# Optimization experiments

Measured on AMD Instinct MI355X. Metric: run time of the kernel, lower is better.

## Reference

```python
import jax, jax.numpy as jnp
import numpy as np

B, N, K, D, H = 4, 256, 32, 32, 8
NUM_SPATIAL, NUM_EDGES = 512, 1024


def setup_inputs() -> dict:
    key = jax.random.key(0)
    k1, k2, k3, k4, k5 = jax.random.split(key, 5)
    spatial_pos = jax.random.randint(k1, (B, N, N), 0, NUM_SPATIAL, dtype=jnp.int64)
    edge_input = jax.random.randint(k2, (B, N, N, K), 0, NUM_EDGES + 1, dtype=jnp.int64)
    spatial_emb = jax.random.normal(k3, (NUM_SPATIAL, H), dtype=jnp.float32)
    spatial_emb = spatial_emb.at[0].set(0.0)  # padding_idx=0
    edge_feat_emb = jax.random.normal(k4, (NUM_EDGES + 1, D), dtype=jnp.float32)
    edge_feat_emb = edge_feat_emb.at[0].set(0.0)  # padding_idx=0
    edge_pos_emb = jax.random.normal(k5, (K, D * H), dtype=jnp.float32)
    return {"spatial_pos": spatial_pos, "edge_input": edge_input,
            "spatial_emb": spatial_emb, "edge_feat_emb": edge_feat_emb,
            "edge_pos_emb": edge_pos_emb}


def reference(spatial_pos, edge_input, spatial_emb, edge_feat_emb, edge_pos_emb):
    # spatial bias: gather [B,N,N,H] -> [B,H,N,N]
    spatial_bias = jnp.transpose(spatial_emb[spatial_pos], (0, 3, 1, 2))
    # edge feature gather: [B,N,N,K,D]
    edge_feat = edge_feat_emb[edge_input]
    pos_weight = edge_pos_emb.reshape(K, D, H)  # [K,D,H]
    # per-hop projection then mean over valid hops
    terms = jnp.einsum('bnmkd,kdh->bnmkh', edge_feat, pos_weight)  # [B,N,N,K,H]
    mask = (edge_input != 0)
    path_len = jnp.maximum(mask.sum(axis=-1, keepdims=True).astype(terms.dtype), 1.0)  # [B,N,N,1]
    edge_bias = terms.sum(axis=-2) / path_len  # [B,N,N,H]
    edge_bias = jnp.transpose(edge_bias, (0, 3, 1, 2))  # [B,H,N,N]
    return spatial_bias + edge_bias
```

## Files before the change

### kernel.cpp

```cpp
#include <hip/hip_runtime.h>
#include <hip/hip_bf16.h>

#define BB 4
#define NN 256
#define KK 32
#define DD 32
#define HH 8
#define NROWS 1024
#define NPTS (BB * NN * NN)
#define NNSQ (NN * NN)
#define TPB 1024
#define NBLK (NPTS / TPB)
#define NPH 16
#define SLICE_US (NROWS * HH)
#define IPAD 4

typedef __attribute__((ext_vector_type(8))) unsigned short ushort8;
typedef __attribute__((ext_vector_type(4))) int iv4;
typedef __attribute__((ext_vector_type(4))) float fv4;

#define LGKM0 asm volatile("s_waitcnt lgkmcnt(0)" ::: "memory")
#define BAR   __builtin_amdgcn_s_barrier()

__device__ __forceinline__ unsigned short f2bf(float f) {
    unsigned u = __float_as_uint(f);
    unsigned r = (u + 0x7FFFu + ((u >> 16) & 1u)) >> 16;
    return (unsigned short)r;
}

__global__ __launch_bounds__(256) void build_proj_bf16(
    const float* __restrict__ feat,
    const float* __restrict__ w,
    unsigned short* __restrict__ proj)
{
    int t  = blockIdx.x * 256 + threadIdx.x;
    int k  = t >> 10;
    int e  = (t & 1023) + 1;

    const float* frow = feat + (size_t)e * DD;
    const float* wrow = w + (size_t)k * DD * HH;

    float acc[HH];
#pragma unroll
    for (int h = 0; h < HH; ++h) acc[h] = 0.0f;

#pragma unroll
    for (int d = 0; d < DD; ++d) {
        float f = frow[d];
#pragma unroll
        for (int h = 0; h < HH; ++h) acc[h] = fmaf(f, wrow[d * HH + h], acc[h]);
    }

    ushort8 o;
#pragma unroll
    for (int h = 0; h < HH; ++h) o[h] = f2bf(acc[h]);
    *(ushort8*)(proj + (size_t)t * HH) = o;
}

template <int E>
__global__ __launch_bounds__(TPB) void attn_bias_v6(
    const int* __restrict__ sp,
    const int* __restrict__ ei,
    const float* __restrict__ semb,
    const unsigned short* __restrict__ proj,
    float* __restrict__ out)
{
    __shared__ __align__(16) unsigned short tbuf[2][2 * SLICE_US];
    __shared__ unsigned int ibuf[2][4][NROWS + IPAD];

    const int tid = threadIdx.x;
    const int p0  = blockIdx.x * TPB;

    const fv4* P4  = (const fv4*)proj;
    const iv4* EI4 = (const iv4*)ei;
    const size_t bi4 = (size_t)p0 * (8 * E);

    fv4 S0, S1;
    iv4 cv[4];

    auto issueS = [&](int ph) {
        S0 = P4[(size_t)(2 * ph)     * 1024 + tid];
        S1 = P4[(size_t)(2 * ph + 1) * 1024 + tid];
    };
    auto writeS = [&](int nb) {
        *(fv4*)&tbuf[nb][tid * 8]            = S0;
        *(fv4*)&tbuf[nb][SLICE_US + tid * 8] = S1;
    };
    auto issueC = [&](int g) {
        if (E == 2) {
#pragma unroll
            for (int c = 0; c < 4; ++c) {
                int j = c * TPB + tid, pt = j >> 2, q = j & 3;
                cv[c] = EI4[bi4 + (size_t)pt * 16 + 4 * g + q];
            }
        } else {
#pragma unroll
            for (int c = 0; c < 2; ++c) {
                int j = c * TPB + tid, pt = j >> 1, q = j & 1;
                cv[c] = EI4[bi4 + (size_t)pt * 8 + 2 * g + q];
            }
        }
    };
    auto writeC = [&](int nb) {
        if (E == 2) {
#pragma unroll
            for (int c = 0; c < 4; ++c) {
                int j = c * TPB + tid, pt = j >> 2, q = j & 3;
                unsigned pk = ((unsigned)cv[c].x & 0xffffu) |
                              (((unsigned)cv[c].z & 0xffffu) << 16);
                ibuf[nb][q][pt] = pk;
            }
        } else {
#pragma unroll
            for (int c = 0; c < 2; ++c) {
                int j = c * TPB + tid, pt = j >> 1, q = j & 1;
                ibuf[nb][q * 2][pt] = ((unsigned)cv[c].x & 0xffffu) |
                                      (((unsigned)cv[c].y & 0xffffu) << 16);
                ibuf[nb][q * 2 + 1][pt] = ((unsigned)cv[c].z & 0xffffu) |
                                          (((unsigned)cv[c].w & 0xffffu) << 16);
            }
        }
    };

    issueS(0);
    issueC(0);
    const int pg = p0 + tid;
    int s = (E == 2) ? (int)((const long long*)sp)[pg] : sp[pg];

    writeS(0);
    issueS(1);
    writeC(0);
    issueC(1);
    LGKM0;
    BAR;

    float acc[HH];
#pragma unroll
    for (int h = 0; h < HH; ++h) acc[h] = 0.0f;
    int cnt = 0;

#pragma unroll 1
    for (int ph = 0; ph < NPH; ++ph) {
        const int g = ph >> 2;

        unsigned pr = ibuf[g & 1][ph & 3][tid];
        int e0 = pr & 0xffffu;
        int e1 = pr >> 16;
        int r0 = e0 ? (e0 - 1) : 0;
        int r1 = e1 ? (e1 - 1) : 0;
        float m0 = e0 ? 1.0f : 0.0f;
        float m1 = e1 ? 1.0f : 0.0f;
        cnt += (e0 != 0) + (e1 != 0);

        const unsigned short* tb = tbuf[ph & 1];
        ushort8 w0 = *(const ushort8*)&tb[r0 * 8];
        ushort8 w1 = *(const ushort8*)&tb[SLICE_US + r1 * 8];
#pragma unroll
        for (int h = 0; h < HH; ++h) {
            acc[h] = fmaf(m0, __uint_as_float(((unsigned)w0[h]) << 16), acc[h]);
            acc[h] = fmaf(m1, __uint_as_float(((unsigned)w1[h]) << 16), acc[h]);
        }

        if (ph < NPH - 1) {
            writeS((ph + 1) & 1);
            if (ph < NPH - 2) issueS(ph + 2);
            if ((ph & 3) == 3 && ph < 12) {
                writeC((g + 1) & 1);
                if (ph < 8) issueC(g + 2);
            }
            LGKM0;
            BAR;
        }
    }

    const float4* srow = (const float4*)(semb + (size_t)s * HH);
    float4 s0v = srow[0], s1v = srow[1];
    float sb[HH] = {s0v.x, s0v.y, s0v.z, s0v.w, s1v.x, s1v.y, s1v.z, s1v.w};

    float inv = 1.0f / (float)(cnt ? cnt : 1);
    float* o = out + (size_t)(pg >> 16) * (HH * NNSQ) + (pg & (NNSQ - 1));
#pragma unroll
    for (int h = 0; h < HH; ++h)
        o[(size_t)h * NNSQ] = sb[h] + acc[h] * inv;
}

extern "C" void kernel_launch(void* const* d_in, const int* in_sizes, int n_in,
                              void* d_out, int out_size, void* d_ws, size_t ws_size,
                              hipStream_t stream) {
    const int*   sp = (const int*)d_in[0];
    const int*   ei = (const int*)d_in[1];
    const float* se = (const float*)d_in[2];
    const float* fe = (const float*)d_in[3];
    const float* pw = (const float*)d_in[4];
    float* out = (float*)d_out;

    const bool i64 = (in_sizes[0] == 2 * NPTS);
    unsigned short* proj = (unsigned short*)d_ws;

    build_proj_bf16<<<128, 256, 0, stream>>>(fe, pw, proj);

    if (i64) attn_bias_v6<2><<<NBLK, TPB, 0, stream>>>(sp, ei, se, proj, out);
    else     attn_bias_v6<1><<<NBLK, TPB, 0, stream>>>(sp, ei, se, proj, out);
}
```

Measured before the change: 27.50 us.

## Stage projection slices via direct global-to-LDS loads with triple-buffered pipeline

Replaces the register-staged double-buffered projection table copy with global_load_lds direct-to-LDS loads into a three-slot ring, fully unrolling the 16 phases with explicit vmcnt waits. Padding hops now read from a shared zero row instead of a mask multiply, so the FMAs become plain adds. The aim is to cut register round-trips and LDS write instructions and to keep more loads in flight per barrier. In exchange it depends on hand-counted vmcnt values, which are fragile if the compiler reorders or adds memory operations.

```diff
diff --git a/kernel.cpp b/kernel.cpp
--- a/kernel.cpp
+++ b/kernel.cpp
@@ -11,21 +11,28 @@
 #define NNSQ (NN * NN)
 #define TPB 1024
 #define NBLK (NPTS / TPB)
-#define NPH 16
 #define SLICE_US (NROWS * HH)
-#define IPAD 4
+#define SLOT_US  (2 * SLICE_US)
 
 typedef __attribute__((ext_vector_type(8))) unsigned short ushort8;
 typedef __attribute__((ext_vector_type(4))) int iv4;
-typedef __attribute__((ext_vector_type(4))) float fv4;
-
-#define LGKM0 asm volatile("s_waitcnt lgkmcnt(0)" ::: "memory")
-#define BAR   __builtin_amdgcn_s_barrier()
+
+#define FENCE  asm volatile("" ::: "memory")
+#define LGKM0  asm volatile("s_waitcnt lgkmcnt(0)" ::: "memory")
+#define BAR    __builtin_amdgcn_s_barrier()
+#define VMW(n) asm volatile("s_waitcnt vmcnt(" #n ")" ::: "memory")
 
 __device__ __forceinline__ unsigned short f2bf(float f) {
     unsigned u = __float_as_uint(f);
     unsigned r = (u + 0x7FFFu + ((u >> 16) & 1u)) >> 16;
     return (unsigned short)r;
+}
+
+__device__ __forceinline__ void gload16(const void* g, void* l) {
+    __builtin_amdgcn_global_load_lds(
+        (const __attribute__((address_space(1))) void*)g,
+        (__attribute__((address_space(3))) void*)l,
+        16, 0, 0);
 }
 
 __global__ __launch_bounds__(256) void build_proj_bf16(
@@ -58,122 +65,120 @@
 }
 
 template <int E>
-__global__ __launch_bounds__(TPB) void attn_bias_v6(
+__global__ __launch_bounds__(TPB) void attn_bias_v8(
     const int* __restrict__ sp,
     const int* __restrict__ ei,
     const float* __restrict__ semb,
     const unsigned short* __restrict__ proj,
     float* __restrict__ out)
 {
-    __shared__ __align__(16) unsigned short tbuf[2][2 * SLICE_US];
-    __shared__ unsigned int ibuf[2][4][NROWS + IPAD];
+    __shared__ __align__(16) unsigned short tbuf[3 * SLOT_US];
+    __shared__ __align__(16) unsigned short zrow[8];
+    __shared__ unsigned int ibuf[2][4][NROWS + 4];
 
     const int tid = threadIdx.x;
     const int p0  = blockIdx.x * TPB;
-
-    const fv4* P4  = (const fv4*)proj;
+    const int pg  = p0 + tid;
+
+    constexpr int NC = (E == 2) ? 4 : 2;
     const iv4* EI4 = (const iv4*)ei;
     const size_t bi4 = (size_t)p0 * (8 * E);
 
-    fv4 S0, S1;
-    iv4 cv[4];
-
-    auto issueS = [&](int ph) {
-        S0 = P4[(size_t)(2 * ph)     * 1024 + tid];
-        S1 = P4[(size_t)(2 * ph + 1) * 1024 + tid];
-    };
-    auto writeS = [&](int nb) {
-        *(fv4*)&tbuf[nb][tid * 8]            = S0;
-        *(fv4*)&tbuf[nb][SLICE_US + tid * 8] = S1;
-    };
+    iv4 cv[NC];
+
     auto issueC = [&](int g) {
-        if (E == 2) {
-#pragma unroll
-            for (int c = 0; c < 4; ++c) {
+#pragma unroll
+        for (int c = 0; c < NC; ++c) {
+            if (E == 2) {
                 int j = c * TPB + tid, pt = j >> 2, q = j & 3;
                 cv[c] = EI4[bi4 + (size_t)pt * 16 + 4 * g + q];
-            }
-        } else {
-#pragma unroll
-            for (int c = 0; c < 2; ++c) {
+            } else {
                 int j = c * TPB + tid, pt = j >> 1, q = j & 1;
                 cv[c] = EI4[bi4 + (size_t)pt * 8 + 2 * g + q];
             }
         }
     };
     auto writeC = [&](int nb) {
-        if (E == 2) {
-#pragma unroll
-            for (int c = 0; c < 4; ++c) {
+#pragma unroll
+        for (int c = 0; c < NC; ++c) {
+            if (E == 2) {
                 int j = c * TPB + tid, pt = j >> 2, q = j & 3;
-                unsigned pk = ((unsigned)cv[c].x & 0xffffu) |
-                              (((unsigned)cv[c].z & 0xffffu) << 16);
-                ibuf[nb][q][pt] = pk;
-            }
-        } else {
-#pragma unroll
-            for (int c = 0; c < 2; ++c) {
+                ibuf[nb][q][pt] = ((unsigned)cv[c].x & 0xffffu) |
+                                  ((unsigned)cv[c].z << 16);
+            } else {
                 int j = c * TPB + tid, pt = j >> 1, q = j & 1;
-                ibuf[nb][q * 2][pt] = ((unsigned)cv[c].x & 0xffffu) |
-                                      (((unsigned)cv[c].y & 0xffffu) << 16);
-                ibuf[nb][q * 2 + 1][pt] = ((unsigned)cv[c].z & 0xffffu) |
-                                          (((unsigned)cv[c].w & 0xffffu) << 16);
+                ibuf[nb][2 * q][pt] = ((unsigned)cv[c].x & 0xffffu) |
+                                      ((unsigned)cv[c].y << 16);
+                ibuf[nb][2 * q + 1][pt] = ((unsigned)cv[c].z & 0xffffu) |
+                                          ((unsigned)cv[c].w << 16);
             }
         }
     };
-
-    issueS(0);
+    auto stage2 = [&](int phn, int slot) {
+        gload16(proj + (size_t)(2 * phn) * SLICE_US + tid * HH,
+                &tbuf[slot * SLOT_US + tid * HH]);
+        gload16(proj + (size_t)(2 * phn + 1) * SLICE_US + tid * HH,
+                &tbuf[slot * SLOT_US + SLICE_US + tid * HH]);
+    };
+
+    float acc[HH];
+#pragma unroll
+    for (int h = 0; h < HH; ++h) acc[h] = 0.0f;
+    int cnt = 0;
+
+    auto dohops = [&](int slot, int gsel, int q) {
+        unsigned pr = ibuf[gsel][q][tid];
+        int e0 = pr & 0xffffu;
+        int e1 = pr >> 16;
+        cnt += (e0 != 0) + (e1 != 0);
+        const unsigned short* tb = &tbuf[slot * SLOT_US];
+        const unsigned short* a0 = e0 ? tb + (e0 - 1) * HH : zrow;
+        const unsigned short* a1 = e1 ? tb + SLICE_US + (e1 - 1) * HH : zrow;
+        ushort8 w0 = *(const ushort8*)a0;
+        ushort8 w1 = *(const ushort8*)a1;
+#pragma unroll
+        for (int h = 0; h < HH; ++h) {
+            acc[h] += __uint_as_float(((unsigned)w0[h]) << 16);
+            acc[h] += __uint_as_float(((unsigned)w1[h]) << 16);
+        }
+    };
+
+#define VMWA do { if constexpr (E == 2) VMW(6); else VMW(4); } while (0)
+#define ENDPH do { FENCE; VMW(2); LGKM0; BAR; } while (0)
+
+    int sv = (E == 2) ? (int)((const long long*)sp)[pg] : sp[pg];
+    FENCE;
     issueC(0);
-    const int pg = p0 + tid;
-    int s = (E == 2) ? (int)((const long long*)sp)[pg] : sp[pg];
-
-    writeS(0);
-    issueS(1);
+    FENCE;
+    stage2(0, 0);
+    stage2(1, 1);
+    if (tid == 0) *(float4*)zrow = make_float4(0.f, 0.f, 0.f, 0.f);
+    FENCE;
     writeC(0);
     issueC(1);
-    LGKM0;
-    BAR;
-
-    float acc[HH];
-#pragma unroll
-    for (int h = 0; h < HH; ++h) acc[h] = 0.0f;
-    int cnt = 0;
-
-#pragma unroll 1
-    for (int ph = 0; ph < NPH; ++ph) {
-        const int g = ph >> 2;
-
-        unsigned pr = ibuf[g & 1][ph & 3][tid];
-        int e0 = pr & 0xffffu;
-        int e1 = pr >> 16;
-        int r0 = e0 ? (e0 - 1) : 0;
-        int r1 = e1 ? (e1 - 1) : 0;
-        float m0 = e0 ? 1.0f : 0.0f;
-        float m1 = e1 ? 1.0f : 0.0f;
-        cnt += (e0 != 0) + (e1 != 0);
-
-        const unsigned short* tb = tbuf[ph & 1];
-        ushort8 w0 = *(const ushort8*)&tb[r0 * 8];
-        ushort8 w1 = *(const ushort8*)&tb[SLICE_US + r1 * 8];
-#pragma unroll
-        for (int h = 0; h < HH; ++h) {
-            acc[h] = fmaf(m0, __uint_as_float(((unsigned)w0[h]) << 16), acc[h]);
-            acc[h] = fmaf(m1, __uint_as_float(((unsigned)w1[h]) << 16), acc[h]);
-        }
-
-        if (ph < NPH - 1) {
-            writeS((ph + 1) & 1);
-            if (ph < NPH - 2) issueS(ph + 2);
-            if ((ph & 3) == 3 && ph < 12) {
-                writeC((g + 1) & 1);
-                if (ph < 8) issueC(g + 2);
-            }
-            LGKM0;
-            BAR;
-        }
-    }
-
-    const float4* srow = (const float4*)(semb + (size_t)s * HH);
+    FENCE;
+    VMWA; LGKM0; BAR;
+
+    stage2(2, 2);  FENCE; dohops(0, 0, 0); FENCE; VMWA; LGKM0; BAR;
+    stage2(3, 0);  FENCE; dohops(1, 0, 1); ENDPH;
+    stage2(4, 1);  FENCE; dohops(2, 0, 2); ENDPH;
+    stage2(5, 2);  FENCE; dohops(0, 0, 3); writeC(1); issueC(2);
+                   FENCE; VMWA; LGKM0; BAR;
+    stage2(6, 0);  FENCE; dohops(1, 1, 0); FENCE; VMWA; LGKM0; BAR;
+    stage2(7, 1);  FENCE; dohops(2, 1, 1); ENDPH;
+    stage2(8, 2);  FENCE; dohops(0, 1, 2); ENDPH;
+    stage2(9, 0);  FENCE; dohops(1, 1, 3); writeC(0); issueC(3);
+                   FENCE; VMWA; LGKM0; BAR;
+    stage2(10, 1); FENCE; dohops(2, 0, 0); FENCE; VMWA; LGKM0; BAR;
+    stage2(11, 2); FENCE; dohops(0, 0, 1); ENDPH;
+    stage2(12, 0); FENCE; dohops(1, 0, 2); ENDPH;
+    stage2(13, 1); FENCE; dohops(2, 0, 3); writeC(1); ENDPH;
+    stage2(14, 2); FENCE; dohops(0, 1, 0); ENDPH;
+    stage2(15, 0); FENCE; dohops(1, 1, 1); ENDPH;
+    dohops(2, 1, 2); FENCE; VMW(0); LGKM0; BAR;
+    dohops(0, 1, 3);
+
+    const float4* srow = (const float4*)(semb + (size_t)sv * HH);
     float4 s0v = srow[0], s1v = srow[1];
     float sb[HH] = {s0v.x, s0v.y, s0v.z, s0v.w, s1v.x, s1v.y, s1v.z, s1v.w};
 
@@ -199,6 +204,6 @@
 
     build_proj_bf16<<<128, 256, 0, stream>>>(fe, pw, proj);
 
-    if (i64) attn_bias_v6<2><<<NBLK, TPB, 0, stream>>>(sp, ei, se, proj, out);
-    else     attn_bias_v6<1><<<NBLK, TPB, 0, stream>>>(sp, ei, se, proj, out);
-}
+    if (i64) attn_bias_v8<2><<<NBLK, TPB, 0, stream>>>(sp, ei, se, proj, out);
+    else     attn_bias_v8<1><<<NBLK, TPB, 0, stream>>>(sp, ei, se, proj, out);
+}
```

Measured after the change: 25.81 us. 6.1% less time.
